# Kernel tuning notes

Measured on AMD Instinct MI355X. Metric: run time of the kernel, lower is better.

The kernel has to match this reference:

```python
import jax, jax.numpy as jnp
import numpy as np

B, C = 32768, 1000

def setup_inputs() -> dict:
    key = jax.random.key(0)
    k1, k2 = jax.random.split(key)
    pred = jax.random.normal(k1, (B, C), dtype=jnp.float32)
    target = jax.random.randint(k2, (B,), 0, C, dtype=jnp.int64)
    return {"pred": pred, "target": target}

def reference(pred, target):
    b, c = pred.shape
    # histogram of labels: replaces the per-class Python loop
    class_freq = jnp.zeros((c,), dtype=pred.dtype).at[target].add(1.0)
    # exp(pred) * freq, then log-normalize over classes (balanced softmax)
    scaled = jnp.exp(pred) * class_freq  # [B, C]
    log_norm = jnp.log(jnp.sum(scaled, axis=1, keepdims=True))  # [B, 1]
    logits = jnp.log(scaled) - log_norm  # [B, C]
    # one-hot multiply + sum == gather logit at target class
    picked = jnp.take_along_axis(logits, target[:, None], axis=1)  # [B, 1]
    return -jnp.sum(picked) / b
```

## Files before the change

kernel.cpp:

```cpp
#include <hip/hip_runtime.h>

#define B_ROWS 32768
#define C_COLS 1000
#define NF4 250
#define MAIN_BLOCKS 2048
#define WAVES_TOTAL (MAIN_BLOCKS * 4)

__global__ __launch_bounds__(256) void bsl_hist(const int* __restrict__ target,
                                                float* __restrict__ freq) {
    __shared__ unsigned int lh[C_COLS];
    const int tid = threadIdx.x;
    for (int i = tid; i < C_COLS; i += 256) lh[i] = 0u;
    __syncthreads();
    const int4* t4 = reinterpret_cast<const int4*>(target + blockIdx.x * 2048);
    #pragma unroll
    for (int k = 0; k < 2; ++k) {
        int4 v = t4[tid + k * 256];
        atomicAdd(&lh[v.x], 1u);
        atomicAdd(&lh[v.y], 1u);
        atomicAdd(&lh[v.z], 1u);
        atomicAdd(&lh[v.w], 1u);
    }
    __syncthreads();
    for (int i = tid; i < C_COLS; i += 256) {
        unsigned int c = lh[i];
        if (c) atomicAdd(&freq[i], (float)c);
    }
}

__global__ __launch_bounds__(256) void bsl_main(const float* __restrict__ pred,
                                                const int* __restrict__ target,
                                                const float* __restrict__ freq,
                                                float* __restrict__ partials) {
    __shared__ float sfreq[C_COLS];
    __shared__ float swave[4];
    const int tid = threadIdx.x;
    const int lane = tid & 63;
    const int wib = tid >> 6;

    for (int i = tid; i < C_COLS; i += 256) sfreq[i] = freq[i];
    __syncthreads();
    const float4* sf4 = reinterpret_cast<const float4*>(sfreq);

    const int gwid = blockIdx.x * 4 + wib;
    float local = 0.0f;

    for (int row = gwid; row < B_ROWS; row += WAVES_TOTAL) {
        const int t = target[row];
        const float4* prow = reinterpret_cast<const float4*>(pred + (size_t)row * C_COLS);
        const int t4i = t >> 2, tm = t & 3;
        float partial = 0.0f, pt = 0.0f;
        #pragma unroll
        for (int k = 0; k < 4; ++k) {
            const int j = k * 64 + lane;
            if (j < NF4) {
                const float4 v = prow[j];
                const float4 f = sf4[j];
                partial += __expf(v.x) * f.x + __expf(v.y) * f.y
                         + __expf(v.z) * f.z + __expf(v.w) * f.w;
                if (j == t4i)
                    pt = (tm & 1) ? ((tm & 2) ? v.w : v.y)
                                  : ((tm & 2) ? v.z : v.x);
            }
        }
        #pragma unroll
        for (int off = 32; off > 0; off >>= 1)
            partial += __shfl_xor(partial, off, 64);
        const float ptb = __shfl(pt, t4i & 63, 64);
        local += logf(partial) - ptb - logf(sfreq[t]);
    }

    if (lane == 0) swave[wib] = local;
    __syncthreads();
    if (tid == 0)
        partials[blockIdx.x] = swave[0] + swave[1] + swave[2] + swave[3];
}

__global__ __launch_bounds__(256) void bsl_finalize(const float* __restrict__ partials,
                                                    float* __restrict__ out) {
    const int tid = threadIdx.x;
    float s = 0.0f;
    for (int i = tid; i < MAIN_BLOCKS; i += 256) s += partials[i];
    #pragma unroll
    for (int off = 32; off > 0; off >>= 1) s += __shfl_xor(s, off, 64);
    __shared__ float sw[4];
    if ((tid & 63) == 0) sw[tid >> 6] = s;
    __syncthreads();
    if (tid == 0) out[0] = (sw[0] + sw[1] + sw[2] + sw[3]) / (float)B_ROWS;
}

extern "C" void kernel_launch(void* const* d_in, const int* in_sizes, int n_in,
                              void* d_out, int out_size, void* d_ws, size_t ws_size,
                              hipStream_t stream) {
    const float* pred = (const float*)d_in[0];
    const int* target = (const int*)d_in[1];

    float* freq     = (float*)d_ws;
    float* partials = freq + 1024;

    hipMemsetAsync(freq, 0, 1024 * sizeof(float), stream);

    bsl_hist<<<16, 256, 0, stream>>>(target, freq);
    bsl_main<<<MAIN_BLOCKS, 256, 0, stream>>>(pred, target, freq, partials);
    bsl_finalize<<<1, 256, 0, stream>>>(partials, (float*)d_out);
}
```

Baseline: 36.75 us.

## Drop memset and global atomics in histogram; load two rows per wave at once

The histogram kernel now writes per-block partial counts to workspace, and every main block sums the 16 partials into shared memory. This removes the memset launch and the global float atomics. The main kernel gives each wave exactly four rows, handled two at a time, with both rows' loads issued before the exp/accumulate work to raise memory-level parallelism. The cost is that every block reads 16x more frequency data, and the hardcoded row count per wave assumes a fixed grid covering all rows.

```diff
diff --git a/kernel.cpp b/kernel.cpp
--- a/kernel.cpp
+++ b/kernel.cpp
@@ -3,11 +3,11 @@
 #define B_ROWS 32768
 #define C_COLS 1000
 #define NF4 250
+#define HIST_BLOCKS 16
 #define MAIN_BLOCKS 2048
-#define WAVES_TOTAL (MAIN_BLOCKS * 4)
 
 __global__ __launch_bounds__(256) void bsl_hist(const int* __restrict__ target,
-                                                float* __restrict__ freq) {
+                                                float* __restrict__ freq_part) {
     __shared__ unsigned int lh[C_COLS];
     const int tid = threadIdx.x;
     for (int i = tid; i < C_COLS; i += 256) lh[i] = 0u;
@@ -22,15 +22,13 @@
         atomicAdd(&lh[v.w], 1u);
     }
     __syncthreads();
-    for (int i = tid; i < C_COLS; i += 256) {
-        unsigned int c = lh[i];
-        if (c) atomicAdd(&freq[i], (float)c);
-    }
+    float* dst = freq_part + blockIdx.x * C_COLS;
+    for (int i = tid; i < C_COLS; i += 256) dst[i] = (float)lh[i];
 }
 
 __global__ __launch_bounds__(256) void bsl_main(const float* __restrict__ pred,
                                                 const int* __restrict__ target,
-                                                const float* __restrict__ freq,
+                                                const float* __restrict__ freq_part,
                                                 float* __restrict__ partials) {
     __shared__ float sfreq[C_COLS];
     __shared__ float swave[4];
@@ -38,36 +36,69 @@
     const int lane = tid & 63;
     const int wib = tid >> 6;
 
-    for (int i = tid; i < C_COLS; i += 256) sfreq[i] = freq[i];
+    for (int i = tid; i < C_COLS; i += 256) {
+        float s = 0.0f;
+        #pragma unroll
+        for (int b = 0; b < HIST_BLOCKS; ++b) s += freq_part[b * C_COLS + i];
+        sfreq[i] = s;
+    }
     __syncthreads();
     const float4* sf4 = reinterpret_cast<const float4*>(sfreq);
 
-    const int gwid = blockIdx.x * 4 + wib;
+    const int base = (blockIdx.x * 4 + wib) * 4;
     float local = 0.0f;
 
-    for (int row = gwid; row < B_ROWS; row += WAVES_TOTAL) {
-        const int t = target[row];
-        const float4* prow = reinterpret_cast<const float4*>(pred + (size_t)row * C_COLS);
-        const int t4i = t >> 2, tm = t & 3;
-        float partial = 0.0f, pt = 0.0f;
+    #pragma unroll
+    for (int p = 0; p < 2; ++p) {
+        const int r0 = base + p * 2;
+        const int r1 = r0 + 1;
+        const int t0 = target[r0], t1 = target[r1];
+        const float4* p0 = reinterpret_cast<const float4*>(pred + (size_t)r0 * C_COLS);
+        const float4* p1 = reinterpret_cast<const float4*>(pred + (size_t)r1 * C_COLS);
+        const int t4i0 = t0 >> 2, tm0 = t0 & 3;
+        const int t4i1 = t1 >> 2, tm1 = t1 & 3;
+
+        float4 v0[4], v1[4];
+        #pragma unroll
+        for (int k = 0; k < 4; ++k) {
+            const int j = k * 64 + lane;
+            if (j < NF4) v0[k] = p0[j];
+        }
+        #pragma unroll
+        for (int k = 0; k < 4; ++k) {
+            const int j = k * 64 + lane;
+            if (j < NF4) v1[k] = p1[j];
+        }
+
+        float s0 = 0.0f, s1 = 0.0f, pt0 = 0.0f, pt1 = 0.0f;
         #pragma unroll
         for (int k = 0; k < 4; ++k) {
             const int j = k * 64 + lane;
             if (j < NF4) {
-                const float4 v = prow[j];
                 const float4 f = sf4[j];
-                partial += __expf(v.x) * f.x + __expf(v.y) * f.y
-                         + __expf(v.z) * f.z + __expf(v.w) * f.w;
-                if (j == t4i)
-                    pt = (tm & 1) ? ((tm & 2) ? v.w : v.y)
-                                  : ((tm & 2) ? v.z : v.x);
+                const float4 a = v0[k];
+                const float4 b = v1[k];
+                s0 += __expf(a.x) * f.x + __expf(a.y) * f.y
+                    + __expf(a.z) * f.z + __expf(a.w) * f.w;
+                s1 += __expf(b.x) * f.x + __expf(b.y) * f.y
+                    + __expf(b.z) * f.z + __expf(b.w) * f.w;
+                if (j == t4i0)
+                    pt0 = (tm0 & 1) ? ((tm0 & 2) ? a.w : a.y)
+                                    : ((tm0 & 2) ? a.z : a.x);
+                if (j == t4i1)
+                    pt1 = (tm1 & 1) ? ((tm1 & 2) ? b.w : b.y)
+                                    : ((tm1 & 2) ? b.z : b.x);
             }
         }
         #pragma unroll
-        for (int off = 32; off > 0; off >>= 1)
-            partial += __shfl_xor(partial, off, 64);
-        const float ptb = __shfl(pt, t4i & 63, 64);
-        local += logf(partial) - ptb - logf(sfreq[t]);
+        for (int off = 32; off > 0; off >>= 1) {
+            s0 += __shfl_xor(s0, off, 64);
+            s1 += __shfl_xor(s1, off, 64);
+        }
+        const float ptb0 = __shfl(pt0, t4i0 & 63, 64);
+        const float ptb1 = __shfl(pt1, t4i1 & 63, 64);
+        local += logf(s0) - ptb0 - logf(sfreq[t0]);
+        local += logf(s1) - ptb1 - logf(sfreq[t1]);
     }
 
     if (lane == 0) swave[wib] = local;
@@ -95,12 +126,10 @@
     const float* pred = (const float*)d_in[0];
     const int* target = (const int*)d_in[1];
 
-    float* freq     = (float*)d_ws;
-    float* partials = freq + 1024;
+    float* freq_part = (float*)d_ws;
+    float* partials  = freq_part + HIST_BLOCKS * C_COLS;
 
-    hipMemsetAsync(freq, 0, 1024 * sizeof(float), stream);
-
-    bsl_hist<<<16, 256, 0, stream>>>(target, freq);
-    bsl_main<<<MAIN_BLOCKS, 256, 0, stream>>>(pred, target, freq, partials);
+    bsl_hist<<<HIST_BLOCKS, 256, 0, stream>>>(target, freq_part);
+    bsl_main<<<MAIN_BLOCKS, 256, 0, stream>>>(pred, target, freq_part, partials);
     bsl_finalize<<<1, 256, 0, stream>>>(partials, (float*)d_out);
 }
```

Result: slower. 39.84 us (+8.4%).

## Drop memset and finalize launch via redundant per-block histogram and last-block reduction

Applied to the files above, without the earlier changes.

Each histogram block now counts all targets in shared memory and writes its own slice of bins directly. This removes the memset and the global float atomics. The finalize kernel is merged into the main kernel using an atomic counter, so the last finishing block reduces the partials. The goal is fewer launches and less serialization, at the cost of redundant histogram work per block and a threadfence/atomic at the end of every main block.

```diff
diff --git a/kernel.cpp b/kernel.cpp
--- a/kernel.cpp
+++ b/kernel.cpp
@@ -5,16 +5,20 @@
 #define NF4 250
 #define MAIN_BLOCKS 2048
 #define WAVES_TOTAL (MAIN_BLOCKS * 4)
+#define HIST_BLOCKS 16
+#define BINS_PER_BLOCK 64
 
 __global__ __launch_bounds__(256) void bsl_hist(const int* __restrict__ target,
-                                                float* __restrict__ freq) {
-    __shared__ unsigned int lh[C_COLS];
+                                                float* __restrict__ freq,
+                                                unsigned int* __restrict__ counter) {
+    __shared__ unsigned int lh[1024];
     const int tid = threadIdx.x;
-    for (int i = tid; i < C_COLS; i += 256) lh[i] = 0u;
+    #pragma unroll
+    for (int i = tid; i < 1024; i += 256) lh[i] = 0u;
     __syncthreads();
-    const int4* t4 = reinterpret_cast<const int4*>(target + blockIdx.x * 2048);
-    #pragma unroll
-    for (int k = 0; k < 2; ++k) {
+    const int4* t4 = reinterpret_cast<const int4*>(target);
+    #pragma unroll 8
+    for (int k = 0; k < 32; ++k) {
         int4 v = t4[tid + k * 256];
         atomicAdd(&lh[v.x], 1u);
         atomicAdd(&lh[v.y], 1u);
@@ -22,18 +26,20 @@
         atomicAdd(&lh[v.w], 1u);
     }
     __syncthreads();
-    for (int i = tid; i < C_COLS; i += 256) {
-        unsigned int c = lh[i];
-        if (c) atomicAdd(&freq[i], (float)c);
-    }
+    const int bin = blockIdx.x * BINS_PER_BLOCK + tid;
+    if (tid < BINS_PER_BLOCK && bin < C_COLS) freq[bin] = (float)lh[bin];
+    if (blockIdx.x == 0 && tid == 0) *counter = 0u;
 }
 
 __global__ __launch_bounds__(256) void bsl_main(const float* __restrict__ pred,
                                                 const int* __restrict__ target,
                                                 const float* __restrict__ freq,
-                                                float* __restrict__ partials) {
+                                                float* __restrict__ partials,
+                                                unsigned int* __restrict__ counter,
+                                                float* __restrict__ out) {
     __shared__ float sfreq[C_COLS];
     __shared__ float swave[4];
+    __shared__ bool winner;
     const int tid = threadIdx.x;
     const int lane = tid & 63;
     const int wib = tid >> 6;
@@ -72,21 +78,25 @@
 
     if (lane == 0) swave[wib] = local;
     __syncthreads();
-    if (tid == 0)
+    if (tid == 0) {
         partials[blockIdx.x] = swave[0] + swave[1] + swave[2] + swave[3];
-}
+        __threadfence();
+        unsigned int t = atomicAdd(counter, 1u);
+        winner = (t == MAIN_BLOCKS - 1);
+    }
+    __syncthreads();
 
-__global__ __launch_bounds__(256) void bsl_finalize(const float* __restrict__ partials,
-                                                    float* __restrict__ out) {
-    const int tid = threadIdx.x;
-    float s = 0.0f;
-    for (int i = tid; i < MAIN_BLOCKS; i += 256) s += partials[i];
-    #pragma unroll
-    for (int off = 32; off > 0; off >>= 1) s += __shfl_xor(s, off, 64);
-    __shared__ float sw[4];
-    if ((tid & 63) == 0) sw[tid >> 6] = s;
-    __syncthreads();
-    if (tid == 0) out[0] = (sw[0] + sw[1] + sw[2] + sw[3]) / (float)B_ROWS;
+    if (winner) {
+        __threadfence();
+        float s = 0.0f;
+        for (int i = tid; i < MAIN_BLOCKS; i += 256) s += partials[i];
+        #pragma unroll
+        for (int off = 32; off > 0; off >>= 1) s += __shfl_xor(s, off, 64);
+        if (lane == 0) swave[wib] = s;
+        __syncthreads();
+        if (tid == 0)
+            out[0] = (swave[0] + swave[1] + swave[2] + swave[3]) / (float)B_ROWS;
+    }
 }
 
 extern "C" void kernel_launch(void* const* d_in, const int* in_sizes, int n_in,
@@ -95,12 +105,11 @@
     const float* pred = (const float*)d_in[0];
     const int* target = (const int*)d_in[1];
 
-    float* freq     = (float*)d_ws;
-    float* partials = freq + 1024;
+    float* freq            = (float*)d_ws;
+    float* partials        = freq + 1024;
+    unsigned int* counter  = (unsigned int*)(partials + MAIN_BLOCKS);
 
-    hipMemsetAsync(freq, 0, 1024 * sizeof(float), stream);
-
-    bsl_hist<<<16, 256, 0, stream>>>(target, freq);
-    bsl_main<<<MAIN_BLOCKS, 256, 0, stream>>>(pred, target, freq, partials);
-    bsl_finalize<<<1, 256, 0, stream>>>(partials, (float*)d_out);
+    bsl_hist<<<HIST_BLOCKS, 256, 0, stream>>>(target, freq, counter);
+    bsl_main<<<MAIN_BLOCKS, 256, 0, stream>>>(pred, target, freq, partials,
+                                              counter, (float*)d_out);
 }
```

New measurement: 83.02 us. 2.26x slower.
